# Kernel optimization log

Measured on AMD Instinct MI355X. Metric: run time of the kernel, lower is better.

The kernel has to match this reference:

```python
import jax, jax.numpy as jnp
import numpy as np

N_NODES = 100_000
N_EDGES = 3_200_000


def setup_inputs() -> dict:
    key = jax.random.key(0)
    ks = jax.random.split(key, 13)
    x_node = jax.random.normal(ks[0], (N_NODES, 32), jnp.float32)
    x_edge = jax.random.normal(ks[1], (N_EDGES, 6), jnp.float32)
    src = jax.random.randint(ks[2], (N_EDGES,), 0, N_NODES)
    dst = jax.random.randint(ks[3], (N_EDGES,), 0, N_NODES)
    b_mask = jax.random.randint(ks[4], (N_EDGES,), 0, 2).astype(jnp.int32)
    s = 0.1  # small init scale for numerical sanity
    Wn1 = jax.random.normal(ks[5], (38, 64), jnp.float32) * s
    bn1 = jax.random.normal(ks[6], (64,), jnp.float32) * s
    Wn2 = jax.random.normal(ks[7], (64, 32), jnp.float32) * s
    bn2 = jax.random.normal(ks[8], (32,), jnp.float32) * s
    We1 = jax.random.normal(ks[9], (70, 32), jnp.float32) * s
    be1 = jax.random.normal(ks[10], (32,), jnp.float32) * s
    We2 = jax.random.normal(ks[11], (32, 6), jnp.float32) * s
    be2 = jax.random.normal(ks[12], (6,), jnp.float32) * s
    return dict(x_node=x_node, x_edge=x_edge, src=src, dst=dst, b_mask=b_mask,
                Wn1=Wn1, bn1=bn1, Wn2=Wn2, bn2=bn2,
                We1=We1, be1=be1, We2=We2, be2=be2)


def reference(x_node, x_edge, src, dst, b_mask,
              Wn1, bn1, Wn2, bn2, We1, be1, We2, be2):
    # Edge messages: forward edges (b_mask==0) use [src, dst, e];
    # backward edges (b_mask==1) use [dst, src, e]. One fused pass.
    back = (b_mask == 1)[:, None]
    xs = x_node[src]                      # [E, 32]
    xd = x_node[dst]                      # [E, 32]
    a = jnp.where(back, xd, xs)
    b = jnp.where(back, xs, xd)
    feat_e = jnp.concatenate([a, b, x_edge], axis=1)          # [E, 70]
    em = jax.nn.relu(feat_e @ We1 + be1) @ We2 + be2          # [E, 6]

    # Node messages: per in-edge, MLP([dst_x, em]); sum into dst node.
    feat_n = jnp.concatenate([xd, em], axis=1)                # [E, 38]
    msg = jax.nn.relu(feat_n @ Wn1 + bn1) @ Wn2 + bn2         # [E, 32]
    nm = jax.ops.segment_sum(msg, dst, num_segments=x_node.shape[0])  # [N, 32]
    return nm, em
```

## Files before the change

### kernel.cpp

```cpp
#include <hip/hip_runtime.h>
#include <hip/hip_bf16.h>

typedef __attribute__((ext_vector_type(8))) short short8;
typedef __attribute__((ext_vector_type(4))) float f32x4;
typedef __attribute__((ext_vector_type(2))) float f32x2;

#define NN 100000
#define NE 3200000

__device__ __forceinline__ short f2bf(float f) {
  __hip_bfloat16 h = __float2bfloat16(f);
  return *reinterpret_cast<short*>(&h);
}

__device__ __forceinline__ f32x4 mfma16(short8 a, short8 b, f32x4 c) {
  return __builtin_amdgcn_mfma_f32_16x16x32_bf16(a, b, c, 0, 0, 0);
}

__global__ void __launch_bounds__(256) mpn_main(
    const float* __restrict__ x_node,
    const float* __restrict__ x_edge,
    const int*   __restrict__ srcp,
    const int*   __restrict__ dstp,
    const int*   __restrict__ bmp,
    const float* __restrict__ Wn1, const float* __restrict__ bn1,
    const float* __restrict__ Wn2, const float* __restrict__ bn2,
    const float* __restrict__ We1, const float* __restrict__ be1,
    const float* __restrict__ We2, const float* __restrict__ be2,
    float* __restrict__ out_nm,
    float* __restrict__ out_em)
{
  __shared__ short lds_h1[4][16][40];
  __shared__ float lds_em[4][16][12];
  __shared__ short lds_h2[4][16][72];

  const int tid  = threadIdx.x;
  const int wid  = tid >> 6;
  const int lane = tid & 63;
  const int col  = lane & 15;
  const int kg   = lane >> 4;

  for (int i = lane; i < 16 * 12; i += 64)
    ((float*)lds_em[wid])[i] = 0.f;

  auto ldb = [&](const float* W, int K, int N, int kc, int nt) {
    int n  = nt * 16 + col;
    int k0 = kc * 32 + kg * 8;
    short8 r;
#pragma unroll
    for (int j = 0; j < 8; ++j) {
      int k = k0 + j;
      float v = (k < K && n < N) ? W[k * N + n] : 0.f;
      r[j] = f2bf(v);
    }
    return r;
  };

  short8 B_e1[3][2], B_n1[2][4], B_n2[2][2], B_e2;
#pragma unroll
  for (int kc = 0; kc < 3; ++kc)
#pragma unroll
    for (int nt = 0; nt < 2; ++nt) B_e1[kc][nt] = ldb(We1, 70, 32, kc, nt);
  B_e2 = ldb(We2, 32, 6, 0, 0);
#pragma unroll
  for (int kc = 0; kc < 2; ++kc)
#pragma unroll
    for (int nt = 0; nt < 4; ++nt) B_n1[kc][nt] = ldb(Wn1, 38, 64, kc, nt);
#pragma unroll
  for (int kc = 0; kc < 2; ++kc)
#pragma unroll
    for (int nt = 0; nt < 2; ++nt) B_n2[kc][nt] = ldb(Wn2, 64, 32, kc, nt);

  float bias_e1[2], bias_n1[4], bias_n2[2], bias_e2;
  bias_e1[0] = be1[col];      bias_e1[1] = be1[16 + col];
  bias_e2    = (col < 6) ? be2[col] : 0.f;
#pragma unroll
  for (int nt = 0; nt < 4; ++nt) bias_n1[nt] = bn1[nt * 16 + col];
  bias_n2[0] = bn2[col];      bias_n2[1] = bn2[16 + col];

  const int ntiles = NE / 16;
  const int gw = blockIdx.x * 4 + wid;
  const int nw = gridDim.x * 4;

  for (int t = gw; t < ntiles; t += nw) {
    const int eb = t * 16;
    const int e  = eb + col;
    const int s  = srcp[e];
    const int d  = dstp[e];
    const bool back = bmp[e] != 0;

    const float* ps = x_node + (long)s * 32 + kg * 8;
    const float* pd = x_node + (long)d * 32 + kg * 8;
    f32x4 s0 = *(const f32x4*)ps, s1 = *(const f32x4*)(ps + 4);
    f32x4 d0 = *(const f32x4*)pd, d1 = *(const f32x4*)(pd + 4);
    short8 XS, XD;
#pragma unroll
    for (int j = 0; j < 4; ++j) {
      XS[j] = f2bf(s0[j]); XS[4 + j] = f2bf(s1[j]);
      XD[j] = f2bf(d0[j]); XD[4 + j] = f2bf(d1[j]);
    }
    short8 AE = {0, 0, 0, 0, 0, 0, 0, 0};
    if (kg == 0) {
      const float* pe = x_edge + (long)e * 6;
      f32x2 e0 = *(const f32x2*)pe;
      f32x2 e1 = *(const f32x2*)(pe + 2);
      f32x2 e2 = *(const f32x2*)(pe + 4);
      AE[0] = f2bf(e0[0]); AE[1] = f2bf(e0[1]);
      AE[2] = f2bf(e1[0]); AE[3] = f2bf(e1[1]);
      AE[4] = f2bf(e2[0]); AE[5] = f2bf(e2[1]);
    }
    short8 Aa = back ? XD : XS;
    short8 Ab = back ? XS : XD;

    f32x4 a0 = {bias_e1[0], bias_e1[0], bias_e1[0], bias_e1[0]};
    f32x4 a1 = {bias_e1[1], bias_e1[1], bias_e1[1], bias_e1[1]};
    a0 = mfma16(Aa, B_e1[0][0], a0);
    a0 = mfma16(Ab, B_e1[1][0], a0);
    a0 = mfma16(AE, B_e1[2][0], a0);
    a1 = mfma16(Aa, B_e1[0][1], a1);
    a1 = mfma16(Ab, B_e1[1][1], a1);
    a1 = mfma16(AE, B_e1[2][1], a1);

#pragma unroll
    for (int r = 0; r < 4; ++r) {
      lds_h1[wid][kg * 4 + r][col]      = f2bf(fmaxf(a0[r], 0.f));
      lds_h1[wid][kg * 4 + r][16 + col] = f2bf(fmaxf(a1[r], 0.f));
    }
    short8 Ah1 = *(const short8*)&lds_h1[wid][col][kg * 8];

    f32x4 ae2 = {bias_e2, bias_e2, bias_e2, bias_e2};
    ae2 = mfma16(Ah1, B_e2, ae2);

    if (col < 6) {
#pragma unroll
      for (int r = 0; r < 4; ++r) {
        int row = kg * 4 + r;
        float v = ae2[r];
        out_em[(long)(eb + row) * 6 + col] = v;
        lds_em[wid][row][col] = v;
      }
    }
    short8 Aem = {0, 0, 0, 0, 0, 0, 0, 0};
    if (kg == 0) {
      f32x4 u0 = *(const f32x4*)&lds_em[wid][col][0];
      f32x4 u1 = *(const f32x4*)&lds_em[wid][col][4];
      Aem[0] = f2bf(u0[0]); Aem[1] = f2bf(u0[1]);
      Aem[2] = f2bf(u0[2]); Aem[3] = f2bf(u0[3]);
      Aem[4] = f2bf(u1[0]); Aem[5] = f2bf(u1[1]);
      Aem[6] = f2bf(u1[2]); Aem[7] = f2bf(u1[3]);
    }

    f32x4 an[4];
#pragma unroll
    for (int nt = 0; nt < 4; ++nt) {
      an[nt] = (f32x4){bias_n1[nt], bias_n1[nt], bias_n1[nt], bias_n1[nt]};
      an[nt] = mfma16(XD,  B_n1[0][nt], an[nt]);
      an[nt] = mfma16(Aem, B_n1[1][nt], an[nt]);
    }
#pragma unroll
    for (int nt = 0; nt < 4; ++nt)
#pragma unroll
      for (int r = 0; r < 4; ++r)
        lds_h2[wid][kg * 4 + r][nt * 16 + col] = f2bf(fmaxf(an[nt][r], 0.f));
    short8 Ah2a = *(const short8*)&lds_h2[wid][col][kg * 8];
    short8 Ah2b = *(const short8*)&lds_h2[wid][col][32 + kg * 8];

    f32x4 am0 = {bias_n2[0], bias_n2[0], bias_n2[0], bias_n2[0]};
    f32x4 am1 = {bias_n2[1], bias_n2[1], bias_n2[1], bias_n2[1]};
    am0 = mfma16(Ah2a, B_n2[0][0], am0);
    am0 = mfma16(Ah2b, B_n2[1][0], am0);
    am1 = mfma16(Ah2a, B_n2[0][1], am1);
    am1 = mfma16(Ah2b, B_n2[1][1], am1);

#pragma unroll
    for (int r = 0; r < 4; ++r) {
      int de = dstp[eb + kg * 4 + r];
      float* basep = out_nm + (long)de * 32 + col;
      unsafeAtomicAdd(basep,      am0[r]);
      unsafeAtomicAdd(basep + 16, am1[r]);
    }
  }
}

extern "C" void kernel_launch(void* const* d_in, const int* in_sizes, int n_in,
                              void* d_out, int out_size, void* d_ws, size_t ws_size,
                              hipStream_t stream) {
  const float* x_node = (const float*)d_in[0];
  const float* x_edge = (const float*)d_in[1];
  const int*   src    = (const int*)d_in[2];
  const int*   dst    = (const int*)d_in[3];
  const int*   bm     = (const int*)d_in[4];
  const float* Wn1 = (const float*)d_in[5];  const float* bn1 = (const float*)d_in[6];
  const float* Wn2 = (const float*)d_in[7];  const float* bn2 = (const float*)d_in[8];
  const float* We1 = (const float*)d_in[9];  const float* be1 = (const float*)d_in[10];
  const float* We2 = (const float*)d_in[11]; const float* be2 = (const float*)d_in[12];
  float* out_nm = (float*)d_out;
  float* out_em = out_nm + (size_t)NN * 32;

  hipMemsetAsync(out_nm, 0, (size_t)NN * 32 * sizeof(float), stream);
  mpn_main<<<1024, 256, 0, stream>>>(x_node, x_edge, src, dst, bm,
                                     Wn1, bn1, Wn2, bn2, We1, be1, We2, be2,
                                     out_nm, out_em);
}
```

Before: 353.6 us.

## Software-pipeline index loads and node gathers across grid-stride tiles

Restructures the grid-stride loop so the next tile's node-feature and edge-feature gathers are issued before the current tile's MLP compute. Indices for the tile after that are prefetched one step further ahead, and the dst indices used by the atomics are loaded early. The grid size is doubled to 2048 blocks. The aim is to hide random-gather latency behind MFMA work, at the cost of extra registers that may lower occupancy.

```diff
diff --git a/kernel.cpp b/kernel.cpp
--- a/kernel.cpp
+++ b/kernel.cpp
@@ -7,6 +7,7 @@
 
 #define NN 100000
 #define NE 3200000
+#define NTILES (NE / 16)
 
 __device__ __forceinline__ short f2bf(float f) {
   __hip_bfloat16 h = __float2bfloat16(f);
@@ -78,37 +79,62 @@
   for (int nt = 0; nt < 4; ++nt) bias_n1[nt] = bn1[nt * 16 + col];
   bias_n2[0] = bn2[col];      bias_n2[1] = bn2[16 + col];
 
-  const int ntiles = NE / 16;
   const int gw = blockIdx.x * 4 + wid;
   const int nw = gridDim.x * 4;
-
-  for (int t = gw; t < ntiles; t += nw) {
-    const int eb = t * 16;
-    const int e  = eb + col;
-    const int s  = srcp[e];
-    const int d  = dstp[e];
-    const bool back = bmp[e] != 0;
-
+  if (gw >= NTILES) return;
+
+  auto ldidx = [&](int t, int& s, int& d, int& b) {
+    int e = t * 16 + col;
+    s = srcp[e]; d = dstp[e]; b = bmp[e];
+  };
+  auto gather = [&](int t, int s, int d,
+                    f32x4& g0, f32x4& g1, f32x4& g2, f32x4& g3,
+                    f32x2& e0, f32x2& e1, f32x2& e2) {
     const float* ps = x_node + (long)s * 32 + kg * 8;
     const float* pd = x_node + (long)d * 32 + kg * 8;
-    f32x4 s0 = *(const f32x4*)ps, s1 = *(const f32x4*)(ps + 4);
-    f32x4 d0 = *(const f32x4*)pd, d1 = *(const f32x4*)(pd + 4);
+    g0 = *(const f32x4*)ps; g1 = *(const f32x4*)(ps + 4);
+    g2 = *(const f32x4*)pd; g3 = *(const f32x4*)(pd + 4);
+    if (kg == 0) {
+      const float* pe = x_edge + (long)(t * 16 + col) * 6;
+      e0 = *(const f32x2*)pe; e1 = *(const f32x2*)(pe + 2); e2 = *(const f32x2*)(pe + 4);
+    }
+  };
+
+  int sI, dI, bI;
+  int tC = gw;
+  ldidx(tC, sI, dI, bI);
+  f32x4 Rs0, Rs1, Rd0, Rd1; f32x2 Re0, Re1, Re2;
+  gather(tC, sI, dI, Rs0, Rs1, Rd0, Rd1, Re0, Re1, Re2);
+  int bR = bI;
+  int tN = gw + nw;
+  { int tc = (tN < NTILES) ? tN : (NTILES - 1); ldidx(tc, sI, dI, bI); }
+
+  while (true) {
+    f32x4 Ns0, Ns1, Nd0, Nd1; f32x2 Ne0, Ne1, Ne2;
+    { int tc = (tN < NTILES) ? tN : (NTILES - 1);
+      gather(tc, sI, dI, Ns0, Ns1, Nd0, Nd1, Ne0, Ne1, Ne2); }
+    int bN = bI;
+    { int t2 = tN + nw; int tc = (t2 < NTILES) ? t2 : (NTILES - 1);
+      ldidx(tc, sI, dI, bI); }
+
+    const int eb = tC * 16;
+    int de[4];
+#pragma unroll
+    for (int r = 0; r < 4; ++r) de[r] = dstp[eb + kg * 4 + r];
+
     short8 XS, XD;
 #pragma unroll
     for (int j = 0; j < 4; ++j) {
-      XS[j] = f2bf(s0[j]); XS[4 + j] = f2bf(s1[j]);
-      XD[j] = f2bf(d0[j]); XD[4 + j] = f2bf(d1[j]);
+      XS[j] = f2bf(Rs0[j]); XS[4 + j] = f2bf(Rs1[j]);
+      XD[j] = f2bf(Rd0[j]); XD[4 + j] = f2bf(Rd1[j]);
     }
     short8 AE = {0, 0, 0, 0, 0, 0, 0, 0};
     if (kg == 0) {
-      const float* pe = x_edge + (long)e * 6;
-      f32x2 e0 = *(const f32x2*)pe;
-      f32x2 e1 = *(const f32x2*)(pe + 2);
-      f32x2 e2 = *(const f32x2*)(pe + 4);
-      AE[0] = f2bf(e0[0]); AE[1] = f2bf(e0[1]);
-      AE[2] = f2bf(e1[0]); AE[3] = f2bf(e1[1]);
-      AE[4] = f2bf(e2[0]); AE[5] = f2bf(e2[1]);
-    }
+      AE[0] = f2bf(Re0[0]); AE[1] = f2bf(Re0[1]);
+      AE[2] = f2bf(Re1[0]); AE[3] = f2bf(Re1[1]);
+      AE[4] = f2bf(Re2[0]); AE[5] = f2bf(Re2[1]);
+    }
+    const bool back = (bR != 0);
     short8 Aa = back ? XD : XS;
     short8 Ab = back ? XS : XD;
 
@@ -174,11 +200,16 @@
 
 #pragma unroll
     for (int r = 0; r < 4; ++r) {
-      int de = dstp[eb + kg * 4 + r];
-      float* basep = out_nm + (long)de * 32 + col;
+      float* basep = out_nm + (long)de[r] * 32 + col;
       unsafeAtomicAdd(basep,      am0[r]);
       unsafeAtomicAdd(basep + 16, am1[r]);
     }
+
+    tC = tN; tN += nw;
+    if (tC >= NTILES) break;
+    Rs0 = Ns0; Rs1 = Ns1; Rd0 = Nd0; Rd1 = Nd1;
+    Re0 = Ne0; Re1 = Ne1; Re2 = Ne2;
+    bR = bN;
   }
 }
 
@@ -198,7 +229,7 @@
   float* out_em = out_nm + (size_t)NN * 32;
 
   hipMemsetAsync(out_nm, 0, (size_t)NN * 32 * sizeof(float), stream);
-  mpn_main<<<1024, 256, 0, stream>>>(x_node, x_edge, src, dst, bm,
+  mpn_main<<<2048, 256, 0, stream>>>(x_node, x_edge, src, dst, bm,
                                      Wn1, bn1, Wn2, bn2, We1, be1, We2, be2,
                                      out_nm, out_em);
 }
```

Measured after the change: 354.0 us. Within noise of the previous version (+0.1%).

## Coalesce node/edge feature gathers through LDS and vectorize em stores

Applied to the files above, without the earlier changes.

Node-feature gathers are restructured so eight lanes cooperatively read one 128-byte row with 16-byte loads, converted to bf16 and staged in LDS, instead of each lane fetching two scattered 32-byte pieces. Edge features and the em output are also moved as contiguous 16-byte vectors per tile through LDS rather than 8-byte per-edge accesses. Destination indices for the atomics now come from a shuffle instead of reloading dstp, and the grid is doubled. The change adds LDS traffic and relies on implicit wave-level ordering of LDS writes and reads without explicit barriers.

```diff
diff --git a/kernel.cpp b/kernel.cpp
--- a/kernel.cpp
+++ b/kernel.cpp
@@ -2,11 +2,14 @@
 #include <hip/hip_bf16.h>
 
 typedef __attribute__((ext_vector_type(8))) short short8;
+typedef __attribute__((ext_vector_type(4))) short s16x4;
+typedef __attribute__((ext_vector_type(4))) int   int4v;
 typedef __attribute__((ext_vector_type(4))) float f32x4;
 typedef __attribute__((ext_vector_type(2))) float f32x2;
 
 #define NN 100000
 #define NE 3200000
+#define NTILES (NE / 16)
 
 __device__ __forceinline__ short f2bf(float f) {
   __hip_bfloat16 h = __float2bfloat16(f);
@@ -30,8 +33,10 @@
     float* __restrict__ out_nm,
     float* __restrict__ out_em)
 {
+  __shared__ short lds_x[4][32 * 40];
+  __shared__ short lds_xe[4][104];
   __shared__ short lds_h1[4][16][40];
-  __shared__ float lds_em[4][16][12];
+  __shared__ float lds_emf[4][96];
   __shared__ short lds_h2[4][16][72];
 
   const int tid  = threadIdx.x;
@@ -39,9 +44,8 @@
   const int lane = tid & 63;
   const int col  = lane & 15;
   const int kg   = lane >> 4;
-
-  for (int i = lane; i < 16 * 12; i += 64)
-    ((float*)lds_em[wid])[i] = 0.f;
+  const int srow   = lane >> 3;
+  const int schunk = lane & 7;
 
   auto ldb = [&](const float* W, int K, int N, int kc, int nt) {
     int n  = nt * 16 + col;
@@ -78,36 +82,47 @@
   for (int nt = 0; nt < 4; ++nt) bias_n1[nt] = bn1[nt * 16 + col];
   bias_n2[0] = bn2[col];      bias_n2[1] = bn2[16 + col];
 
-  const int ntiles = NE / 16;
   const int gw = blockIdx.x * 4 + wid;
   const int nw = gridDim.x * 4;
 
-  for (int t = gw; t < ntiles; t += nw) {
+  for (int t = gw; t < NTILES; t += nw) {
     const int eb = t * 16;
     const int e  = eb + col;
     const int s  = srcp[e];
     const int d  = dstp[e];
     const bool back = bmp[e] != 0;
 
-    const float* ps = x_node + (long)s * 32 + kg * 8;
-    const float* pd = x_node + (long)d * 32 + kg * 8;
-    f32x4 s0 = *(const f32x4*)ps, s1 = *(const f32x4*)(ps + 4);
-    f32x4 d0 = *(const f32x4*)pd, d1 = *(const f32x4*)(pd + 4);
-    short8 XS, XD;
-#pragma unroll
-    for (int j = 0; j < 4; ++j) {
-      XS[j] = f2bf(s0[j]); XS[4 + j] = f2bf(s1[j]);
-      XD[j] = f2bf(d0[j]); XD[4 + j] = f2bf(d1[j]);
-    }
+    const int sA = __shfl(s, srow);
+    const int sB = __shfl(s, 8 + srow);
+    const int dA = __shfl(d, srow);
+    const int dB = __shfl(d, 8 + srow);
+    f32x4 vA = *(const f32x4*)(x_node + (long)sA * 32 + schunk * 4);
+    f32x4 vB = *(const f32x4*)(x_node + (long)sB * 32 + schunk * 4);
+    f32x4 vC = *(const f32x4*)(x_node + (long)dA * 32 + schunk * 4);
+    f32x4 vD = *(const f32x4*)(x_node + (long)dB * 32 + schunk * 4);
+    f32x4 vE;
+    if (lane < 24) vE = *(const f32x4*)(x_edge + (long)eb * 6 + lane * 4);
+
+    auto st4 = [&](int row, f32x4 v) {
+      s16x4 p;
+      p[0] = f2bf(v[0]); p[1] = f2bf(v[1]); p[2] = f2bf(v[2]); p[3] = f2bf(v[3]);
+      *(s16x4*)&lds_x[wid][row * 40 + schunk * 4] = p;
+    };
+    st4(srow, vA); st4(8 + srow, vB); st4(16 + srow, vC); st4(24 + srow, vD);
+    if (lane < 24) {
+      s16x4 p;
+      p[0] = f2bf(vE[0]); p[1] = f2bf(vE[1]); p[2] = f2bf(vE[2]); p[3] = f2bf(vE[3]);
+      *(s16x4*)&lds_xe[wid][lane * 4] = p;
+    }
+
+    short8 XS = *(const short8*)&lds_x[wid][col * 40 + kg * 8];
+    short8 XD = *(const short8*)&lds_x[wid][(16 + col) * 40 + kg * 8];
     short8 AE = {0, 0, 0, 0, 0, 0, 0, 0};
     if (kg == 0) {
-      const float* pe = x_edge + (long)e * 6;
-      f32x2 e0 = *(const f32x2*)pe;
-      f32x2 e1 = *(const f32x2*)(pe + 2);
-      f32x2 e2 = *(const f32x2*)(pe + 4);
-      AE[0] = f2bf(e0[0]); AE[1] = f2bf(e0[1]);
-      AE[2] = f2bf(e1[0]); AE[3] = f2bf(e1[1]);
-      AE[4] = f2bf(e2[0]); AE[5] = f2bf(e2[1]);
+      int4v u = { *(const int*)&lds_xe[wid][col * 6],
+                  *(const int*)&lds_xe[wid][col * 6 + 2],
+                  *(const int*)&lds_xe[wid][col * 6 + 4], 0 };
+      AE = __builtin_bit_cast(short8, u);
     }
     short8 Aa = back ? XD : XS;
     short8 Ab = back ? XS : XD;
@@ -133,21 +148,21 @@
 
     if (col < 6) {
 #pragma unroll
-      for (int r = 0; r < 4; ++r) {
-        int row = kg * 4 + r;
-        float v = ae2[r];
-        out_em[(long)(eb + row) * 6 + col] = v;
-        lds_em[wid][row][col] = v;
-      }
+      for (int r = 0; r < 4; ++r)
+        lds_emf[wid][(kg * 4 + r) * 6 + col] = ae2[r];
     }
     short8 Aem = {0, 0, 0, 0, 0, 0, 0, 0};
     if (kg == 0) {
-      f32x4 u0 = *(const f32x4*)&lds_em[wid][col][0];
-      f32x4 u1 = *(const f32x4*)&lds_em[wid][col][4];
+      f32x2 u0 = *(const f32x2*)&lds_emf[wid][col * 6];
+      f32x2 u1 = *(const f32x2*)&lds_emf[wid][col * 6 + 2];
+      f32x2 u2 = *(const f32x2*)&lds_emf[wid][col * 6 + 4];
       Aem[0] = f2bf(u0[0]); Aem[1] = f2bf(u0[1]);
-      Aem[2] = f2bf(u0[2]); Aem[3] = f2bf(u0[3]);
-      Aem[4] = f2bf(u1[0]); Aem[5] = f2bf(u1[1]);
-      Aem[6] = f2bf(u1[2]); Aem[7] = f2bf(u1[3]);
+      Aem[2] = f2bf(u1[0]); Aem[3] = f2bf(u1[1]);
+      Aem[4] = f2bf(u2[0]); Aem[5] = f2bf(u2[1]);
+    }
+    if (lane < 24) {
+      f32x4 w = *(const f32x4*)&lds_emf[wid][lane * 4];
+      *(f32x4*)(out_em + (long)eb * 6 + lane * 4) = w;
     }
 
     f32x4 an[4];
@@ -174,7 +189,7 @@
 
 #pragma unroll
     for (int r = 0; r < 4; ++r) {
-      int de = dstp[eb + kg * 4 + r];
+      int de = __shfl(d, kg * 4 + r);
       float* basep = out_nm + (long)de * 32 + col;
       unsafeAtomicAdd(basep,      am0[r]);
       unsafeAtomicAdd(basep + 16, am1[r]);
@@ -198,7 +213,7 @@
   float* out_em = out_nm + (size_t)NN * 32;
 
   hipMemsetAsync(out_nm, 0, (size_t)NN * 32 * sizeof(float), stream);
-  mpn_main<<<1024, 256, 0, stream>>>(x_node, x_edge, src, dst, bm,
+  mpn_main<<<2048, 256, 0, stream>>>(x_node, x_edge, src, dst, bm,
                                      Wn1, bn1, Wn2, bn2, We1, be1, We2, be2,
                                      out_nm, out_em);
 }
```

Result: slower. 362.8 us (+2.6%).

## Bucket edges by destination and accumulate node messages in shared memory

Applied to the files above, without the earlier changes.

Adds a counting-sort pipeline (histogram, column scan, base scan, scatter) that groups edges into 8192 destination-node buckets, copying src/dst/mask/edge-id and edge features into workspace records. Each wave then processes one bucket, accumulating node messages in LDS and writing out_nm directly. This removes global float atomics and the memset. The cost is extra passes over all edges, a write and read of about 128 MB of records, and possible load imbalance across buckets. A fallback legacy kernel runs when the workspace is too small.

```diff
diff --git a/kernel.cpp b/kernel.cpp
--- a/kernel.cpp
+++ b/kernel.cpp
@@ -2,22 +2,280 @@
 #include <hip/hip_bf16.h>
 
 typedef __attribute__((ext_vector_type(8))) short short8;
+typedef __attribute__((ext_vector_type(4))) int   int4v;
 typedef __attribute__((ext_vector_type(4))) float f32x4;
 typedef __attribute__((ext_vector_type(2))) float f32x2;
 
 #define NN 100000
 #define NE 3200000
+#define NTILES (NE / 16)
+#define NB 8192
+#define NBLK 256
+#define EPB (NE / NBLK)
 
 __device__ __forceinline__ short f2bf(float f) {
   __hip_bfloat16 h = __float2bfloat16(f);
   return *reinterpret_cast<short*>(&h);
 }
-
 __device__ __forceinline__ f32x4 mfma16(short8 a, short8 b, f32x4 c) {
   return __builtin_amdgcn_mfma_f32_16x16x32_bf16(a, b, c, 0, 0, 0);
 }
-
-__global__ void __launch_bounds__(256) mpn_main(
+__device__ __forceinline__ int bucket_of(int d) {
+  return (int)(((unsigned long long)d * NB) / NN);
+}
+
+__global__ void __launch_bounds__(256) k_count(const int* __restrict__ dst,
+                                               int* __restrict__ cnt) {
+  __shared__ int h[NB];
+  for (int j = threadIdx.x; j < NB; j += 256) h[j] = 0;
+  __syncthreads();
+  const int e0 = blockIdx.x * EPB, e1 = e0 + EPB;
+  for (int i = e0 + threadIdx.x; i < e1; i += 256)
+    atomicAdd(&h[bucket_of(dst[i])], 1);
+  __syncthreads();
+  for (int j = threadIdx.x; j < NB; j += 256)
+    cnt[blockIdx.x * NB + j] = h[j];
+}
+
+__global__ void __launch_bounds__(256) k_scan_cols(int* __restrict__ cnt,
+                                                   int* __restrict__ total) {
+  int b = blockIdx.x * 256 + threadIdx.x;
+  if (b >= NB) return;
+  int s = 0;
+  for (int blk = 0; blk < NBLK; ++blk) {
+    int idx = blk * NB + b;
+    int t = cnt[idx];
+    cnt[idx] = s;
+    s += t;
+  }
+  total[b] = s;
+}
+
+__global__ void __launch_bounds__(1024) k_scan_base(const int* __restrict__ total,
+                                                    int* __restrict__ base) {
+  __shared__ int sm[1024];
+  const int tid = threadIdx.x;
+  int t[8], pre[8], cs = 0;
+#pragma unroll
+  for (int k = 0; k < 8; ++k) { t[k] = total[tid * 8 + k]; pre[k] = cs; cs += t[k]; }
+  sm[tid] = cs;
+  __syncthreads();
+  for (int off = 1; off < 1024; off <<= 1) {
+    int x = (tid >= off) ? sm[tid - off] : 0;
+    __syncthreads();
+    sm[tid] += x;
+    __syncthreads();
+  }
+  int excl = sm[tid] - cs;
+#pragma unroll
+  for (int k = 0; k < 8; ++k) base[tid * 8 + k] = excl + pre[k];
+  if (tid == 1023) base[NB] = sm[1023];
+}
+
+__global__ void __launch_bounds__(256) k_scatter(const int* __restrict__ src,
+                                                 const int* __restrict__ dst,
+                                                 const int* __restrict__ bm,
+                                                 const float* __restrict__ x_edge,
+                                                 const int* __restrict__ cnt,
+                                                 const int* __restrict__ base,
+                                                 int4v* __restrict__ recA,
+                                                 float* __restrict__ recXE) {
+  __shared__ int cur[NB];
+  for (int j = threadIdx.x; j < NB; j += 256)
+    cur[j] = cnt[blockIdx.x * NB + j] + base[j];
+  __syncthreads();
+  const int e0 = blockIdx.x * EPB, e1 = e0 + EPB;
+  for (int i = e0 + threadIdx.x; i < e1; i += 256) {
+    int d = dst[i];
+    int b = bucket_of(d);
+    int p = atomicAdd(&cur[b], 1);
+    int4v ra = { src[i] | (bm[i] << 30), d, i, 0 };
+    recA[p] = ra;
+    const f32x2* xs = (const f32x2*)(x_edge + (size_t)i * 6);
+    f32x2* xd = (f32x2*)(recXE + (size_t)p * 6);
+    xd[0] = xs[0]; xd[1] = xs[1]; xd[2] = xs[2];
+  }
+}
+
+__global__ void __launch_bounds__(256) mpn_bucket(
+    const float* __restrict__ x_node,
+    const int4v* __restrict__ recA,
+    const float* __restrict__ recXE,
+    const int*   __restrict__ base,
+    const float* __restrict__ Wn1, const float* __restrict__ bn1,
+    const float* __restrict__ Wn2, const float* __restrict__ bn2,
+    const float* __restrict__ We1, const float* __restrict__ be1,
+    const float* __restrict__ We2, const float* __restrict__ be2,
+    float* __restrict__ out_nm,
+    float* __restrict__ out_em)
+{
+  __shared__ short lds_h1[4][16][40];
+  __shared__ float lds_emf[4][96];
+  __shared__ short lds_h2[4][16][72];
+  __shared__ float accum[4][13 * 32];
+
+  const int tid  = threadIdx.x;
+  const int wid  = tid >> 6;
+  const int lane = tid & 63;
+  const int col  = lane & 15;
+  const int kg   = lane >> 4;
+
+  for (int i = lane; i < 13 * 32; i += 64) accum[wid][i] = 0.f;
+
+  auto ldb = [&](const float* W, int K, int N, int kc, int nt) {
+    int n  = nt * 16 + col;
+    int k0 = kc * 32 + kg * 8;
+    short8 r;
+#pragma unroll
+    for (int j = 0; j < 8; ++j) {
+      int k = k0 + j;
+      float v = (k < K && n < N) ? W[k * N + n] : 0.f;
+      r[j] = f2bf(v);
+    }
+    return r;
+  };
+
+  short8 B_e1[3][2], B_n1[2][4], B_n2[2][2], B_e2;
+#pragma unroll
+  for (int kc = 0; kc < 3; ++kc)
+#pragma unroll
+    for (int nt = 0; nt < 2; ++nt) B_e1[kc][nt] = ldb(We1, 70, 32, kc, nt);
+  B_e2 = ldb(We2, 32, 6, 0, 0);
+#pragma unroll
+  for (int kc = 0; kc < 2; ++kc)
+#pragma unroll
+    for (int nt = 0; nt < 4; ++nt) B_n1[kc][nt] = ldb(Wn1, 38, 64, kc, nt);
+#pragma unroll
+  for (int kc = 0; kc < 2; ++kc)
+#pragma unroll
+    for (int nt = 0; nt < 2; ++nt) B_n2[kc][nt] = ldb(Wn2, 64, 32, kc, nt);
+
+  float bias_e1[2], bias_n1[4], bias_n2[2], bias_e2;
+  bias_e1[0] = be1[col];      bias_e1[1] = be1[16 + col];
+  bias_e2    = (col < 6) ? be2[col] : 0.f;
+#pragma unroll
+  for (int nt = 0; nt < 4; ++nt) bias_n1[nt] = bn1[nt * 16 + col];
+  bias_n2[0] = bn2[col];      bias_n2[1] = bn2[16 + col];
+
+  const int w = blockIdx.x * 4 + wid;
+  if (w >= NB) return;
+  const int n0 = (int)(((long long)w * NN + NB - 1) / NB);
+  const int n1 = (int)(((long long)(w + 1) * NN + NB - 1) / NB);
+  const int win = n1 - n0;
+  const int s0 = base[w], s1 = base[w + 1];
+  const int ntl = (s1 - s0 + 15) >> 4;
+
+  for (int ti = 0; ti < ntl; ++ti) {
+    const int tb  = s0 + ti * 16;
+    const int rem = min(16, s1 - tb);
+    const int rp  = (col < rem) ? (tb + col) : (s1 - 1);
+
+    int4v ra = recA[rp];
+    const int s    = ra.x & 0x3FFFFFFF;
+    const bool back = (ra.x >> 30) & 1;
+    const int d    = ra.y;
+    const int eid  = ra.z;
+
+    const float* ps = x_node + (long)s * 32 + kg * 8;
+    const float* pd = x_node + (long)d * 32 + kg * 8;
+    f32x4 s0v = *(const f32x4*)ps, s1v = *(const f32x4*)(ps + 4);
+    f32x4 d0v = *(const f32x4*)pd, d1v = *(const f32x4*)(pd + 4);
+    short8 XS, XD;
+#pragma unroll
+    for (int j = 0; j < 4; ++j) {
+      XS[j] = f2bf(s0v[j]); XS[4 + j] = f2bf(s1v[j]);
+      XD[j] = f2bf(d0v[j]); XD[4 + j] = f2bf(d1v[j]);
+    }
+    short8 AE = {0, 0, 0, 0, 0, 0, 0, 0};
+    if (kg == 0) {
+      const f32x2* pe = (const f32x2*)(recXE + (size_t)rp * 6);
+      f32x2 e0 = pe[0], e1 = pe[1], e2 = pe[2];
+      AE[0] = f2bf(e0[0]); AE[1] = f2bf(e0[1]);
+      AE[2] = f2bf(e1[0]); AE[3] = f2bf(e1[1]);
+      AE[4] = f2bf(e2[0]); AE[5] = f2bf(e2[1]);
+    }
+    short8 Aa = back ? XD : XS;
+    short8 Ab = back ? XS : XD;
+
+    f32x4 a0 = {bias_e1[0], bias_e1[0], bias_e1[0], bias_e1[0]};
+    f32x4 a1 = {bias_e1[1], bias_e1[1], bias_e1[1], bias_e1[1]};
+    a0 = mfma16(Aa, B_e1[0][0], a0);
+    a0 = mfma16(Ab, B_e1[1][0], a0);
+    a0 = mfma16(AE, B_e1[2][0], a0);
+    a1 = mfma16(Aa, B_e1[0][1], a1);
+    a1 = mfma16(Ab, B_e1[1][1], a1);
+    a1 = mfma16(AE, B_e1[2][1], a1);
+
+#pragma unroll
+    for (int r = 0; r < 4; ++r) {
+      lds_h1[wid][kg * 4 + r][col]      = f2bf(fmaxf(a0[r], 0.f));
+      lds_h1[wid][kg * 4 + r][16 + col] = f2bf(fmaxf(a1[r], 0.f));
+    }
+    short8 Ah1 = *(const short8*)&lds_h1[wid][col][kg * 8];
+
+    f32x4 ae2 = {bias_e2, bias_e2, bias_e2, bias_e2};
+    ae2 = mfma16(Ah1, B_e2, ae2);
+
+#pragma unroll
+    for (int r = 0; r < 4; ++r) {
+      int row = kg * 4 + r;
+      if (col < 6) lds_emf[wid][row * 6 + col] = ae2[r];
+    }
+#pragma unroll
+    for (int r = 0; r < 4; ++r) {
+      int row = kg * 4 + r;
+      int eidr = __shfl(eid, row);
+      if (col < 6 && row < rem)
+        out_em[(long)eidr * 6 + col] = ae2[r];
+    }
+    short8 Aem = {0, 0, 0, 0, 0, 0, 0, 0};
+    if (kg == 0) {
+      f32x2 u0 = *(const f32x2*)&lds_emf[wid][col * 6];
+      f32x2 u1 = *(const f32x2*)&lds_emf[wid][col * 6 + 2];
+      f32x2 u2 = *(const f32x2*)&lds_emf[wid][col * 6 + 4];
+      Aem[0] = f2bf(u0[0]); Aem[1] = f2bf(u0[1]);
+      Aem[2] = f2bf(u1[0]); Aem[3] = f2bf(u1[1]);
+      Aem[4] = f2bf(u2[0]); Aem[5] = f2bf(u2[1]);
+    }
+
+    f32x4 an[4];
+#pragma unroll
+    for (int nt = 0; nt < 4; ++nt) {
+      an[nt] = (f32x4){bias_n1[nt], bias_n1[nt], bias_n1[nt], bias_n1[nt]};
+      an[nt] = mfma16(XD,  B_n1[0][nt], an[nt]);
+      an[nt] = mfma16(Aem, B_n1[1][nt], an[nt]);
+    }
+#pragma unroll
+    for (int nt = 0; nt < 4; ++nt)
+#pragma unroll
+      for (int r = 0; r < 4; ++r)
+        lds_h2[wid][kg * 4 + r][nt * 16 + col] = f2bf(fmaxf(an[nt][r], 0.f));
+    short8 Ah2a = *(const short8*)&lds_h2[wid][col][kg * 8];
+    short8 Ah2b = *(const short8*)&lds_h2[wid][col][32 + kg * 8];
+
+    f32x4 am0 = {bias_n2[0], bias_n2[0], bias_n2[0], bias_n2[0]};
+    f32x4 am1 = {bias_n2[1], bias_n2[1], bias_n2[1], bias_n2[1]};
+    am0 = mfma16(Ah2a, B_n2[0][0], am0);
+    am0 = mfma16(Ah2b, B_n2[1][0], am0);
+    am1 = mfma16(Ah2a, B_n2[0][1], am1);
+    am1 = mfma16(Ah2b, B_n2[1][1], am1);
+
+#pragma unroll
+    for (int r = 0; r < 4; ++r) {
+      int row = kg * 4 + r;
+      if (row < rem) {
+        int dloc = __shfl(d, row) - n0;
+        atomicAdd(&accum[wid][dloc * 32 + col],      am0[r]);
+        atomicAdd(&accum[wid][dloc * 32 + 16 + col], am1[r]);
+      }
+    }
+  }
+
+  for (int rr = (lane >> 5); rr < win; rr += 2)
+    out_nm[(long)(n0 + rr) * 32 + (lane & 31)] = accum[wid][rr * 32 + (lane & 31)];
+}
+
+__global__ void __launch_bounds__(256) mpn_legacy(
     const float* __restrict__ x_node,
     const float* __restrict__ x_edge,
     const int*   __restrict__ srcp,
@@ -31,7 +289,7 @@
     float* __restrict__ out_em)
 {
   __shared__ short lds_h1[4][16][40];
-  __shared__ float lds_em[4][16][12];
+  __shared__ float lds_emf[4][96];
   __shared__ short lds_h2[4][16][72];
 
   const int tid  = threadIdx.x;
@@ -40,9 +298,6 @@
   const int col  = lane & 15;
   const int kg   = lane >> 4;
 
-  for (int i = lane; i < 16 * 12; i += 64)
-    ((float*)lds_em[wid])[i] = 0.f;
-
   auto ldb = [&](const float* W, int K, int N, int kc, int nt) {
     int n  = nt * 16 + col;
     int k0 = kc * 32 + kg * 8;
@@ -78,11 +333,10 @@
   for (int nt = 0; nt < 4; ++nt) bias_n1[nt] = bn1[nt * 16 + col];
   bias_n2[0] = bn2[col];      bias_n2[1] = bn2[16 + col];
 
-  const int ntiles = NE / 16;
   const int gw = blockIdx.x * 4 + wid;
   const int nw = gridDim.x * 4;
 
-  for (int t = gw; t < ntiles; t += nw) {
+  for (int t = gw; t < NTILES; t += nw) {
     const int eb = t * 16;
     const int e  = eb + col;
     const int s  = srcp[e];
@@ -137,17 +391,17 @@
         int row = kg * 4 + r;
         float v = ae2[r];
         out_em[(long)(eb + row) * 6 + col] = v;
-        lds_em[wid][row][col] = v;
+        lds_emf[wid][row * 6 + col] = v;
       }
     }
     short8 Aem = {0, 0, 0, 0, 0, 0, 0, 0};
     if (kg == 0) {
-      f32x4 u0 = *(const f32x4*)&lds_em[wid][col][0];
-      f32x4 u1 = *(const f32x4*)&lds_em[wid][col][4];
+      f32x2 u0 = *(const f32x2*)&lds_emf[wid][col * 6];
+      f32x2 u1 = *(const f32x2*)&lds_emf[wid][col * 6 + 2];
+      f32x2 u2 = *(const f32x2*)&lds_emf[wid][col * 6 + 4];
       Aem[0] = f2bf(u0[0]); Aem[1] = f2bf(u0[1]);
-      Aem[2] = f2bf(u0[2]); Aem[3] = f2bf(u0[3]);
-      Aem[4] = f2bf(u1[0]); Aem[5] = f2bf(u1[1]);
-      Aem[6] = f2bf(u1[2]); Aem[7] = f2bf(u1[3]);
+      Aem[2] = f2bf(u1[0]); Aem[3] = f2bf(u1[1]);
+      Aem[4] = f2bf(u2[0]); Aem[5] = f2bf(u2[1]);
     }
 
     f32x4 an[4];
@@ -174,7 +428,7 @@
 
 #pragma unroll
     for (int r = 0; r < 4; ++r) {
-      int de = dstp[eb + kg * 4 + r];
+      int de = __shfl(d, kg * 4 + r);
       float* basep = out_nm + (long)de * 32 + col;
       unsafeAtomicAdd(basep,      am0[r]);
       unsafeAtomicAdd(basep + 16, am1[r]);
@@ -197,8 +451,32 @@
   float* out_nm = (float*)d_out;
   float* out_em = out_nm + (size_t)NN * 32;
 
-  hipMemsetAsync(out_nm, 0, (size_t)NN * 32 * sizeof(float), stream);
-  mpn_main<<<1024, 256, 0, stream>>>(x_node, x_edge, src, dst, bm,
-                                     Wn1, bn1, Wn2, bn2, We1, be1, We2, be2,
-                                     out_nm, out_em);
-}
+  const size_t o_cnt   = 0;
+  const size_t o_total = o_cnt + (size_t)NBLK * NB * 4;
+  const size_t o_base  = o_total + (size_t)NB * 4;
+  const size_t o_recA  = o_base + 32784;
+  const size_t o_recXE = o_recA + (size_t)NE * 16;
+  const size_t need    = o_recXE + (size_t)NE * 24;
+
+  if (ws_size >= need) {
+    char* w = (char*)d_ws;
+    int*   cnt   = (int*)(w + o_cnt);
+    int*   total = (int*)(w + o_total);
+    int*   base  = (int*)(w + o_base);
+    int4v* recA  = (int4v*)(w + o_recA);
+    float* recXE = (float*)(w + o_recXE);
+
+    k_count<<<NBLK, 256, 0, stream>>>(dst, cnt);
+    k_scan_cols<<<NB / 256, 256, 0, stream>>>(cnt, total);
+    k_scan_base<<<1, 1024, 0, stream>>>(total, base);
+    k_scatter<<<NBLK, 256, 0, stream>>>(src, dst, bm, x_edge, cnt, base, recA, recXE);
+    mpn_bucket<<<NB / 4, 256, 0, stream>>>(x_node, recA, recXE, base,
+                                           Wn1, bn1, Wn2, bn2, We1, be1, We2, be2,
+                                           out_nm, out_em);
+  } else {
+    hipMemsetAsync(out_nm, 0, (size_t)NN * 32 * sizeof(float), stream);
+    mpn_legacy<<<2048, 256, 0, stream>>>(x_node, x_edge, src, dst, bm,
+                                         Wn1, bn1, Wn2, bn2, We1, be1, We2, be2,
+                                         out_nm, out_em);
+  }
+}
```

Measured after the change: 852.0 us. 141% more time.
